# Performance work log

Measured on AMD Instinct MI355X. Metric: run time of the kernel, lower is better.

## Reference

```python
import jax, jax.numpy as jnp
import numpy as np

NUM_HEADS = 8
EPS_OT = 0.05    # self.eps
BETA_T = 1.0     # self.beta_t
N_ITERS = 100    # Sinkhorn max_iter (reference runs all iterations; torch breaks early on convergence)


def setup_inputs() -> dict:
    key = jax.random.key(0)
    ks = jax.random.split(key, 10)
    B, N1, N2 = 16, 256, 576
    dim_t, dim_v, dim_out = 512, 512, 512
    s = 0.02  # conv1d k=1 init scale (stand-in for torch default init)
    f32 = jnp.float32
    return {
        "F_t": jax.random.normal(ks[0], (B, N1, dim_t), f32),
        "F_s": jax.random.normal(ks[1], (B, N2, dim_v), f32),
        # Conv1d(kernel_size=1) weights, squeezed to [out, in]; biases default-on in nn.Conv1d
        "Wq": jax.random.normal(ks[2], (dim_out, dim_t), f32) * s,
        "bq": jnp.zeros((dim_out,), f32),
        "Wk": jax.random.normal(ks[3], (dim_out, dim_v), f32) * s,
        "bk": jnp.zeros((dim_out,), f32),
        "Wv": jax.random.normal(ks[4], (dim_out, dim_v), f32) * s,
        "bv": jnp.zeros((dim_out,), f32),
        "Wp": jax.random.normal(ks[5], (dim_out, dim_out), f32) * s,
        "bp": jnp.zeros((dim_out,), f32),
    }


def sinkhorn_log_exp_sum(C, log_mu, log_nu, eps):
    # C: [BH, N1, N2]; fixed-length log-domain Sinkhorn.
    BH, N1, N2 = C.shape
    u0 = jnp.zeros((BH, N1), C.dtype)
    v0 = jnp.zeros((BH, N2), C.dtype)

    def body(carry, _):
        u, v = carry
        # single K per iteration; both u and v updates use the OLD (u, v), matching torch code
        K = (-C + u[:, :, None] + v[:, None, :]) / eps
        u_new = eps * (log_mu - jax.scipy.special.logsumexp(K, axis=2)) + u
        v_new = eps * (log_nu - jax.scipy.special.logsumexp(K, axis=1)) + v
        return (u_new, v_new), None

    (u, v), _ = jax.lax.scan(jax.checkpoint(body), (u0, v0), None, length=N_ITERS)
    return jnp.exp((-C + u[:, :, None] + v[:, None, :]) / eps)


def _l2norm(x, eps=1e-12):
    return x / jnp.maximum(jnp.linalg.norm(x, axis=-1, keepdims=True), eps)


def reference(F_t, F_s, Wq, bq, Wk, bk, Wv, bv, Wp, bp):
    B, N1, _ = F_t.shape
    N2 = F_s.shape[1]
    H = NUM_HEADS
    dim_out = Wq.shape[0]
    hd = dim_out // H

    # Conv1d(kernel=1) == pointwise linear over channel dim
    q = (F_t @ Wq.T + bq).reshape(B, N1, H, hd)
    k = (F_s @ Wk.T + bk).reshape(B, N2, H, hd)
    v = (F_s @ Wv.T + bv).reshape(B, N2, H, hd)

    q = _l2norm(q)
    k = _l2norm(k)

    sim = jnp.einsum('bnkc,bmkc->bknm', q, k) * BETA_T  # [B,H,N1,N2]
    wdist = (1.0 - sim).reshape(B * H, N1, N2)
    sim_f = sim.reshape(B * H, N1, N2)

    log_mu = jnp.log(jnp.asarray(1.0 / N1 + 1e-8, sim.dtype))
    log_nu = jnp.log(jnp.asarray(1.0 / N2 + 1e-8, sim.dtype))
    T = sinkhorn_log_exp_sum(wdist, log_mu, log_nu, EPS_OT)

    score_map = (N1 * N2 * sim_f * T).reshape(B, H, N1, N2)  # attn_drop = identity (p=0)
    F_t_a = jnp.einsum('bknm,bmkc->bnkc', score_map, v).reshape(B, N1, dim_out)
    F_t_a = F_t_a @ Wp.T + bp
    # torch: F_t_a / F_t_a.norm(dim=-1, keepdim=True)  (plain division, no eps clamp)
    F_t_a = F_t_a / jnp.linalg.norm(F_t_a, axis=-1, keepdims=True)
    return F_t_a  # proj_drop = identity (p=0)
```

## Files before the change

### kernel.cpp

```cpp
#include <hip/hip_runtime.h>
#include <math.h>

#define EPS_OT 0.05f
#define INV_EPS 20.0f

typedef unsigned short ushort_t;
typedef __attribute__((ext_vector_type(8))) short short8;
typedef __attribute__((ext_vector_type(4))) float f32x4;
union Pk { uint4 u; short8 s; };

__device__ __forceinline__ unsigned int f2bf(float f) {
  unsigned int u = __float_as_uint(f);
  return (u + 0x7FFFu + ((u >> 16) & 1u)) >> 16;
}
__device__ __forceinline__ float bf2f(unsigned int u) { return __uint_as_float(u << 16); }

__device__ __forceinline__ void bar_lds() {
  asm volatile("s_waitcnt lgkmcnt(0)" ::: "memory");
  __builtin_amdgcn_s_barrier();
  asm volatile("" ::: "memory");
}

__global__ __launch_bounds__(256) void pack_k(const float* __restrict__ F_t,
                                              const float* __restrict__ F_s,
                                              const float* __restrict__ Wq,
                                              const float* __restrict__ Wk,
                                              const float* __restrict__ Wv,
                                              const float* __restrict__ Wp,
                                              ushort_t* __restrict__ Fth, ushort_t* __restrict__ Ftl,
                                              ushort_t* __restrict__ Fsh, ushort_t* __restrict__ Fsl,
                                              ushort_t* __restrict__ Wqh, ushort_t* __restrict__ Wql,
                                              ushort_t* __restrict__ Wkh, ushort_t* __restrict__ Wkl,
                                              ushort_t* __restrict__ Wvh, ushort_t* __restrict__ Wvl,
                                              ushort_t* __restrict__ Wph) {
  const int blk = blockIdx.x;
  const float* src; ushort_t* dh; ushort_t* dl; size_t off;
  if (blk < 2048)      { src = F_t; dh = Fth; dl = Ftl; off = (size_t)blk * 1024; }
  else if (blk < 6656) { src = F_s; dh = Fsh; dl = Fsl; off = (size_t)(blk - 2048) * 1024; }
  else if (blk < 6912) { src = Wq;  dh = Wqh; dl = Wql; off = (size_t)(blk - 6656) * 1024; }
  else if (blk < 7168) { src = Wk;  dh = Wkh; dl = Wkl; off = (size_t)(blk - 6912) * 1024; }
  else if (blk < 7424) { src = Wv;  dh = Wvh; dl = Wvl; off = (size_t)(blk - 7168) * 1024; }
  else                 { src = Wp;  dh = Wph; dl = nullptr; off = (size_t)(blk - 7424) * 1024; }
  const size_t i = off + (size_t)threadIdx.x * 4;
  float4 f = *(const float4*)(src + i);
  unsigned int h0 = f2bf(f.x), h1 = f2bf(f.y), h2 = f2bf(f.z), h3 = f2bf(f.w);
  uint2 hh; hh.x = h0 | (h1 << 16); hh.y = h2 | (h3 << 16);
  *(uint2*)(dh + i) = hh;
  if (dl) {
    uint2 ll;
    ll.x = f2bf(f.x - bf2f(h0)) | (f2bf(f.y - bf2f(h1)) << 16);
    ll.y = f2bf(f.z - bf2f(h2)) | (f2bf(f.w - bf2f(h3)) << 16);
    *(uint2*)(dl + i) = ll;
  }
}

#define GEMM_HL_BODY()                                                                      \
  f32x4 acc[4] = {};                                                                        \
  for (int k0 = 0; k0 < 512; k0 += 64) {                                                    \
    uint4 a0 = *(const uint4*)(Xp_h + k0), a1 = *(const uint4*)(Xp_h + k0 + 8);             \
    uint4 b0 = *(const uint4*)(Xp_l + k0), b1 = *(const uint4*)(Xp_l + k0 + 8);             \
    uint4 c0 = *(const uint4*)(Wp_h + k0), c1 = *(const uint4*)(Wp_h + k0 + 8);             \
    uint4 d0 = *(const uint4*)(Wp_l + k0), d1 = *(const uint4*)(Wp_l + k0 + 8);             \
    __syncthreads();                                                                        \
    *(uint4*)&Xh[r][cg * 16] = a0; *(uint4*)&Xh[r][cg * 16 + 8] = a1;                       \
    *(uint4*)&Xl[r][cg * 16] = b0; *(uint4*)&Xl[r][cg * 16 + 8] = b1;                       \
    *(uint4*)&Wh[r][cg * 16] = c0; *(uint4*)&Wh[r][cg * 16 + 8] = c1;                       \
    *(uint4*)&Wl[r][cg * 16] = d0; *(uint4*)&Wl[r][cg * 16 + 8] = d1;                       \
    __syncthreads();                                                                        \
    _Pragma("unroll") for (int kst = 0; kst < 2; ++kst) {                                   \
      short8 ah = *(const short8*)&Xh[16 * w + li][kst * 32 + 8 * lg];                      \
      short8 al = *(const short8*)&Xl[16 * w + li][kst * 32 + 8 * lg];                      \
      _Pragma("unroll") for (int nt = 0; nt < 4; ++nt) {                                    \
        short8 bh = *(const short8*)&Wh[nt * 16 + li][kst * 32 + 8 * lg];                   \
        short8 bl = *(const short8*)&Wl[nt * 16 + li][kst * 32 + 8 * lg];                   \
        acc[nt] = __builtin_amdgcn_mfma_f32_16x16x32_bf16(ah, bh, acc[nt], 0, 0, 0);        \
        acc[nt] = __builtin_amdgcn_mfma_f32_16x16x32_bf16(ah, bl, acc[nt], 0, 0, 0);        \
        acc[nt] = __builtin_amdgcn_mfma_f32_16x16x32_bf16(al, bh, acc[nt], 0, 0, 0);        \
      }                                                                                     \
    }                                                                                       \
  }

#define GEMM_PL_BODY()                                                                      \
  f32x4 acc[4] = {};                                                                        \
  for (int k0 = 0; k0 < 512; k0 += 64) {                                                    \
    uint4 a0 = *(const uint4*)(Xp_h + k0), a1 = *(const uint4*)(Xp_h + k0 + 8);             \
    uint4 c0 = *(const uint4*)(Wp_h + k0), c1 = *(const uint4*)(Wp_h + k0 + 8);             \
    __syncthreads();                                                                        \
    *(uint4*)&Xh[r][cg * 16] = a0; *(uint4*)&Xh[r][cg * 16 + 8] = a1;                       \
    *(uint4*)&Wh[r][cg * 16] = c0; *(uint4*)&Wh[r][cg * 16 + 8] = c1;                       \
    __syncthreads();                                                                        \
    _Pragma("unroll") for (int kst = 0; kst < 2; ++kst) {                                   \
      short8 ah = *(const short8*)&Xh[16 * w + li][kst * 32 + 8 * lg];                      \
      _Pragma("unroll") for (int nt = 0; nt < 4; ++nt) {                                    \
        short8 bh = *(const short8*)&Wh[nt * 16 + li][kst * 32 + 8 * lg];                   \
        acc[nt] = __builtin_amdgcn_mfma_f32_16x16x32_bf16(ah, bh, acc[nt], 0, 0, 0);        \
      }                                                                                     \
    }                                                                                       \
  }

__global__ __launch_bounds__(256) void gemmnorm2_k(const ushort_t* __restrict__ Xg_h,
                                                   const ushort_t* __restrict__ Xg_l,
                                                   const ushort_t* __restrict__ Wg_h,
                                                   const ushort_t* __restrict__ Wg_l,
                                                   const float* __restrict__ bias,
                                                   ushort_t* __restrict__ oh,
                                                   ushort_t* __restrict__ ol, int Nn) {
  __shared__ ushort_t Xh[64][72], Xl[64][72], Wh[64][72], Wl[64][72];
  const int tid = threadIdx.x;
  const int w = tid >> 6, l = tid & 63, li = l & 15, lg = l >> 4;
  const int r = tid >> 2, cg = tid & 3;
  const int m0 = blockIdx.x << 6;
  const int h = blockIdx.y, n0 = h << 6;
  const ushort_t* Xp_h = Xg_h + (size_t)(m0 + r) * 512 + cg * 16;
  const ushort_t* Xp_l = Xg_l + (size_t)(m0 + r) * 512 + cg * 16;
  const ushort_t* Wp_h = Wg_h + (size_t)(n0 + r) * 512 + cg * 16;
  const ushort_t* Wp_l = Wg_l + (size_t)(n0 + r) * 512 + cg * 16;
  GEMM_HL_BODY()
  float v[4][4];
  float ss[4] = {0.f, 0.f, 0.f, 0.f};
#pragma unroll
  for (int nt = 0; nt < 4; ++nt) {
    float bb = bias[n0 + nt * 16 + li];
#pragma unroll
    for (int reg = 0; reg < 4; ++reg) {
      float y = acc[nt][reg] + bb;
      v[nt][reg] = y;
      ss[reg] = fmaf(y, y, ss[reg]);
    }
  }
#pragma unroll
  for (int off = 1; off < 16; off <<= 1)
#pragma unroll
    for (int reg = 0; reg < 4; ++reg) ss[reg] += __shfl_xor(ss[reg], off, 64);
  const int b = m0 / Nn;
  const int nbase = m0 - b * Nn;
  const size_t base = ((size_t)(b * 8 + h) * Nn + nbase + 16 * w + 4 * lg) * 64;
#pragma unroll
  for (int reg = 0; reg < 4; ++reg) {
    float inv = 1.0f / fmaxf(sqrtf(ss[reg]), 1e-12f);
#pragma unroll
    for (int nt = 0; nt < 4; ++nt) {
      float y = v[nt][reg] * inv;
      unsigned int hi = f2bf(y);
      size_t idx = base + (size_t)reg * 64 + nt * 16 + li;
      oh[idx] = (ushort_t)hi;
      ol[idx] = (ushort_t)f2bf(y - bf2f(hi));
    }
  }
}

__global__ __launch_bounds__(256) void gemmtrans2_k(const ushort_t* __restrict__ Xg_h,
                                                    const ushort_t* __restrict__ Wg_h,
                                                    const float* __restrict__ bias,
                                                    ushort_t* __restrict__ vt) {
  __shared__ ushort_t Xh[64][72], Wh[64][72];
  __shared__ ushort_t Vs[64 * 73];
  const int tid = threadIdx.x;
  const int w = tid >> 6, l = tid & 63, li = l & 15, lg = l >> 4;
  const int r = tid >> 2, cg = tid & 3;
  const int m0 = blockIdx.x << 6;
  const int h = blockIdx.y, n0 = h << 6;
  const ushort_t* Xp_h = Xg_h + (size_t)(m0 + r) * 512 + cg * 16;
  const ushort_t* Wp_h = Wg_h + (size_t)(n0 + r) * 512 + cg * 16;
  GEMM_PL_BODY()
#pragma unroll
  for (int nt = 0; nt < 4; ++nt) {
    float bb = bias[n0 + nt * 16 + li];
#pragma unroll
    for (int reg = 0; reg < 4; ++reg)
      Vs[(16 * w + 4 * lg + reg) * 73 + nt * 16 + li] = (ushort_t)f2bf(acc[nt][reg] + bb);
  }
  __syncthreads();
  const int a9 = m0 >> 6;
  const int b = a9 / 9;
  const int nbase = m0 - b * 576;
  const int s = b * 8 + h;
  const int c = tid >> 2, q4 = tid & 3;
  ushort_t tmp[16];
#pragma unroll
  for (int jj = 0; jj < 16; ++jj) tmp[jj] = Vs[(q4 * 16 + jj) * 73 + c];
  ushort_t* op = vt + ((size_t)s * 64 + c) * 576 + nbase + q4 * 16;
  *(uint4*)op = *(uint4*)&tmp[0];
  *(uint4*)(op + 8) = *(uint4*)&tmp[8];
}

__global__ __launch_bounds__(256) void gemmplain_k(const ushort_t* __restrict__ Xg_h,
                                                   const ushort_t* __restrict__ Wg_h,
                                                   const float* __restrict__ bias,
                                                   float* __restrict__ Y) {
  __shared__ ushort_t Xh[64][72], Wh[64][72];
  const int tid = threadIdx.x;
  const int w = tid >> 6, l = tid & 63, li = l & 15, lg = l >> 4;
  const int r = tid >> 2, cg = tid & 3;
  const int m0 = blockIdx.x << 6, n0 = blockIdx.y << 6;
  const ushort_t* Xp_h = Xg_h + (size_t)(m0 + r) * 512 + cg * 16;
  const ushort_t* Wp_h = Wg_h + (size_t)(n0 + r) * 512 + cg * 16;
  GEMM_PL_BODY()
#pragma unroll
  for (int nt = 0; nt < 4; ++nt) {
    float bb = bias[n0 + nt * 16 + li];
#pragma unroll
    for (int reg = 0; reg < 4; ++reg)
      Y[(size_t)(m0 + 16 * w + 4 * lg + reg) * 512 + n0 + nt * 16 + li] = acc[nt][reg] + bb;
  }
}

__global__ __launch_bounds__(256) void simE2_k(const ushort_t* __restrict__ qh,
                                               const ushort_t* __restrict__ ql,
                                               const ushort_t* __restrict__ kh,
                                               const ushort_t* __restrict__ kl,
                                               ushort_t* __restrict__ E) {
  const int s = blockIdx.x, i0 = blockIdx.y << 6, j0 = blockIdx.z << 6;
  const int tid = threadIdx.x;
  const int w = tid >> 6, l = tid & 63, li = l & 15, lg = l >> 4;
  const size_t qoff = ((size_t)s * 256 + i0 + 16 * w + li) * 64 + 8 * lg;
  short8 aH0 = *(const short8*)(qh + qoff), aH1 = *(const short8*)(qh + qoff + 32);
  short8 aL0 = *(const short8*)(ql + qoff), aL1 = *(const short8*)(ql + qoff + 32);
  f32x4 acc[4] = {};
#pragma unroll
  for (int nt = 0; nt < 4; ++nt) {
    const size_t koff = ((size_t)s * 576 + j0 + nt * 16 + li) * 64 + 8 * lg;
    short8 bH0 = *(const short8*)(kh + koff), bH1 = *(const short8*)(kh + koff + 32);
    short8 bL0 = *(const short8*)(kl + koff), bL1 = *(const short8*)(kl + koff + 32);
    acc[nt] = __builtin_amdgcn_mfma_f32_16x16x32_bf16(aH0, bH0, acc[nt], 0, 0, 0);
    acc[nt] = __builtin_amdgcn_mfma_f32_16x16x32_bf16(aH1, bH1, acc[nt], 0, 0, 0);
    acc[nt] = __builtin_amdgcn_mfma_f32_16x16x32_bf16(aH0, bL0, acc[nt], 0, 0, 0);
    acc[nt] = __builtin_amdgcn_mfma_f32_16x16x32_bf16(aH1, bL1, acc[nt], 0, 0, 0);
    acc[nt] = __builtin_amdgcn_mfma_f32_16x16x32_bf16(aL0, bH0, acc[nt], 0, 0, 0);
    acc[nt] = __builtin_amdgcn_mfma_f32_16x16x32_bf16(aL1, bH1, acc[nt], 0, 0, 0);
  }
  ushort_t* Ep = E + (size_t)s * 147456;
#pragma unroll
  for (int nt = 0; nt < 4; ++nt)
#pragma unroll
    for (int reg = 0; reg < 4; ++reg) {
      float e = __expf((acc[nt][reg] - 1.0f) * INV_EPS);
      Ep[(size_t)(i0 + 16 * w + 4 * lg + reg) * 576 + j0 + nt * 16 + li] = (ushort_t)f2bf(e);
    }
}

#define SK_SMEM 147456

__global__ __launch_bounds__(1024, 1) void sinkhorn11_k(const ushort_t* __restrict__ E,
                                                        float* __restrict__ gA,
                                                        float* __restrict__ gB,
                                                        unsigned long long* __restrict__ gpart,
                                                        float C_mu, float C_nu) {
  extern __shared__ char smem[];
  const int g = blockIdx.x, s = g >> 1, rh = g & 1, pg = g ^ 1;
  const int tid = threadIdx.x, w = tid >> 6, l = tid & 63, li = l & 15, lg = l >> 4;
  unsigned long long* myP = gpart + (size_t)g * 1152;
  const unsigned long long* prP = gpart + (size_t)pg * 1152;

  ushort_t* Elds = (ushort_t*)smem;
  {
    const uint4* Eg = (const uint4*)(E + (size_t)s * 147456 + (size_t)rh * 73728);
    uint4* El4 = (uint4*)Elds;
    for (int idx = tid; idx < 9216; idx += 1024) El4[idx] = Eg[idx];
  }
  __syncthreads();

  const int art = (w & 7) * 16 + li;
  const int akb = (w >> 3) * 9;
  short8 afr[9];
#pragma unroll
  for (int c = 0; c < 9; ++c)
    afr[c] = *(const short8*)(Elds + art * 576 + (akb + c) * 32 + 8 * lg);

  short8 bfr0, bfr1, bfr2, bfr3, bfr4, bfr5, bfr6, bfr7, bfr8, bfr9, bfr10, bfr11;
#define BFR_BUILD(dst, tc, q)                                                  \
  {                                                                            \
    const ushort_t* p = Elds + ((q) * 32 + 8 * lg) * 576 + (tc) * 16 + li;     \
    Pk pk;                                                                     \
    pk.u.x = (unsigned int)p[0]    | ((unsigned int)p[576]  << 16);            \
    pk.u.y = (unsigned int)p[1152] | ((unsigned int)p[1728] << 16);            \
    pk.u.z = (unsigned int)p[2304] | ((unsigned int)p[2880] << 16);            \
    pk.u.w = (unsigned int)p[3456] | ((unsigned int)p[4032] << 16);            \
    dst = pk.s;                                                                \
  }
  BFR_BUILD(bfr0, w, 0) BFR_BUILD(bfr1, w, 1) BFR_BUILD(bfr2, w, 2) BFR_BUILD(bfr3, w, 3)
  BFR_BUILD(bfr4, w + 16, 0) BFR_BUILD(bfr5, w + 16, 1)
  BFR_BUILD(bfr6, w + 16, 2) BFR_BUILD(bfr7, w + 16, 3)
  if (w < 4) {
    BFR_BUILD(bfr8, w + 32, 0) BFR_BUILD(bfr9, w + 32, 1)
    BFR_BUILD(bfr10, w + 32, 2) BFR_BUILD(bfr11, w + 32, 3)
  } else {
    bfr8 = bfr0; bfr9 = bfr1; bfr10 = bfr2; bfr11 = bfr3;
  }
  __syncthreads();

  float* uu = (float*)smem;
  float* vv = uu + 128;
  ushort_t* au = (ushort_t*)(vv + 576);
  ushort_t* bv = au + 128;
  float* rpart = (float*)(au + 768);
  float* cso = rpart + 256;

  if (tid < 128) { uu[tid] = 0.0f; au[tid] = (ushort_t)0x3F80; }
  if (tid < 576) { vv[tid] = 0.0f; bv[tid] = (ushort_t)0x3F80; }
  __syncthreads();

  const int jj = tid - 128;

  for (int t = 0; t < 100; ++t) {
    const int par = t & 1;
    {
      Pk q0, q1, q2, q3;
      q0.u = *(const uint4*)(au + 8 * lg);
      q1.u = *(const uint4*)(au + 32 + 8 * lg);
      q2.u = *(const uint4*)(au + 64 + 8 * lg);
      q3.u = *(const uint4*)(au + 96 + 8 * lg);
#define MV2_TILE(tc, f0, f1, f2, f3)                                                  \
      {                                                                               \
        f32x4 acc2 = {0.f, 0.f, 0.f, 0.f};                                            \
        acc2 = __builtin_amdgcn_mfma_f32_16x16x32_bf16(q0.s, f0, acc2, 0, 0, 0);      \
        acc2 = __builtin_amdgcn_mfma_f32_16x16x32_bf16(q1.s, f1, acc2, 0, 0, 0);      \
        acc2 = __builtin_amdgcn_mfma_f32_16x16x32_bf16(q2.s, f2, acc2, 0, 0, 0);      \
        acc2 = __builtin_amdgcn_mfma_f32_16x16x32_bf16(q3.s, f3, acc2, 0, 0, 0);      \
        if (l < 16) {                                                                 \
          const int col = (tc) * 16 + l;                                              \
          float cs = acc2[0];                                                         \
          cso[col] = cs;                                                              \
          unsigned long long pv = (unsigned long long)__float_as_uint(cs) |           \
                                  ((unsigned long long)(unsigned int)(t + 1) << 32);  \
          __hip_atomic_store(&myP[par * 576 + col], pv, __ATOMIC_RELAXED,             \
                             __HIP_MEMORY_SCOPE_AGENT);                               \
        }                                                                             \
      }
      MV2_TILE(w, bfr0, bfr1, bfr2, bfr3)
      MV2_TILE(w + 16, bfr4, bfr5, bfr6, bfr7)
      if (w < 4) MV2_TILE(w + 32, bfr8, bfr9, bfr10, bfr11)
    }
    {
      f32x4 acc1 = {0.f, 0.f, 0.f, 0.f};
#pragma unroll
      for (int c = 0; c < 9; ++c) {
        Pk bh; bh.u = *(const uint4*)(bv + (akb + c) * 32 + 8 * lg);
        acc1 = __builtin_amdgcn_mfma_f32_16x16x32_bf16(bh.s, afr[c], acc1, 0, 0, 0);
      }
      if (l < 16) rpart[(w >> 3) * 128 + (w & 7) * 16 + l] = acc1[0];
    }
    bar_lds();
    if (tid < 128) {
      float rs = rpart[tid] + rpart[128 + tid];
      float un = C_mu - EPS_OT * __logf(rs);
      uu[tid] = un;
      au[tid] = (ushort_t)f2bf(__expf(fminf(fmaxf(un * INV_EPS, -80.f), 80.f)));
    } else if (tid < 704) {
      const unsigned int tg = (unsigned int)(t + 1);
      unsigned long long p0;
      for (;;) {
        p0 = __hip_atomic_load(&prP[par * 576 + jj], __ATOMIC_RELAXED, __HIP_MEMORY_SCOPE_AGENT);
        if ((unsigned int)(p0 >> 32) == tg) break;
        __builtin_amdgcn_s_sleep(1);
      }
      float tot = cso[jj] + __uint_as_float((unsigned int)p0);
      float vn = C_nu - EPS_OT * __logf(tot);
      vv[jj] = vn;
      bv[jj] = (ushort_t)f2bf(__expf(fminf(fmaxf(vn * INV_EPS, -80.f), 80.f)));
    }
    bar_lds();
  }
  if (rh == 0 && tid >= 128 && tid < 704) {
    unsigned long long p0;
    for (;;) {
      p0 = __hip_atomic_load(&prP[576 + jj], __ATOMIC_RELAXED, __HIP_MEMORY_SCOPE_AGENT);
      if ((unsigned int)(p0 >> 32) == 100u) break;
      __builtin_amdgcn_s_sleep(1);
    }
    float tot = cso[jj] + __uint_as_float((unsigned int)p0);
    vv[jj] = C_nu - EPS_OT * __logf(tot);
  }
  __syncthreads();
  if (tid < 128) gA[(size_t)s * 256 + rh * 128 + tid] = uu[tid] * INV_EPS;
  if (rh == 0 && tid < 576) gB[(size_t)s * 576 + tid] = vv[tid] * INV_EPS + 11.9012851f;
}

__global__ __launch_bounds__(256) void scorev2_k(const ushort_t* __restrict__ E,
                                                 const ushort_t* __restrict__ vt,
                                                 const float* __restrict__ gA,
                                                 const float* __restrict__ gB,
                                                 ushort_t* __restrict__ Y) {
  __shared__ float gBs[576];
  const int s = blockIdx.x, i0 = blockIdx.y << 6;
  const int tid = threadIdx.x;
  const int w = tid >> 6, l = tid & 63, li = l & 15, lg = l >> 4;
  for (int j = tid; j < 576; j += 256) gBs[j] = gB[(size_t)s * 576 + j];
  const float ga = gA[(size_t)s * 256 + i0 + 16 * w + li];
  const ushort_t* Erow = E + (size_t)s * 147456 + (size_t)(i0 + 16 * w + li) * 576;
  f32x4 acc[4] = {};
  __syncthreads();
  for (int kst = 0; kst < 18; ++kst) {
    const int jb = kst * 32 + 8 * lg;
    Pk eu; eu.u = *(const uint4*)(Erow + jb);
    float pv[8];
#pragma unroll
    for (int jj = 0; jj < 8; ++jj) {
      unsigned int us = (unsigned int)(unsigned short)eu.s[jj];
      float e = bf2f(us);
      float le = __logf(e);
      pv[jj] = (1.0f + EPS_OT * le) * __expf(le + ga + gBs[jb + jj]);
    }
    Pk ph, pl;
#pragma unroll
    for (int jj = 0; jj < 8; ++jj) {
      unsigned int h = f2bf(pv[jj]);
      ((unsigned short*)&ph.s)[jj] = (unsigned short)h;
      ((unsigned short*)&pl.s)[jj] = (unsigned short)f2bf(pv[jj] - bf2f(h));
    }
#pragma unroll
    for (int nt = 0; nt < 4; ++nt) {
      Pk vf; vf.u = *(const uint4*)(vt + ((size_t)s * 64 + nt * 16 + li) * 576 + jb);
      acc[nt] = __builtin_amdgcn_mfma_f32_16x16x32_bf16(ph.s, vf.s, acc[nt], 0, 0, 0);
      acc[nt] = __builtin_amdgcn_mfma_f32_16x16x32_bf16(pl.s, vf.s, acc[nt], 0, 0, 0);
    }
  }
  const int b = s >> 3, h = s & 7;
#pragma unroll
  for (int nt = 0; nt < 4; ++nt)
#pragma unroll
    for (int reg = 0; reg < 4; ++reg)
      Y[((size_t)(b * 256 + i0 + 16 * w + 4 * lg + reg) << 9) + (h << 6) + nt * 16 + li] =
          (ushort_t)f2bf(acc[nt][reg]);
}

__global__ __launch_bounds__(256) void rownorm_k(const float* __restrict__ X,
                                                 float* __restrict__ out) {
  const size_t row = blockIdx.x;
  const int tid = threadIdx.x;
  float x0 = X[(row << 9) + tid], x1 = X[(row << 9) + 256 + tid];
  float st = fmaf(x0, x0, x1 * x1);
#pragma unroll
  for (int off = 32; off; off >>= 1) st += __shfl_xor(st, off, 64);
  __shared__ float ps[4];
  if ((tid & 63) == 0) ps[tid >> 6] = st;
  __syncthreads();
  const float inv = 1.0f / sqrtf(ps[0] + ps[1] + ps[2] + ps[3]);
  out[(row << 9) + tid] = x0 * inv;
  out[(row << 9) + 256 + tid] = x1 * inv;
}

extern "C" void kernel_launch(void* const* d_in, const int* in_sizes, int n_in,
                              void* d_out, int out_size, void* d_ws, size_t ws_size,
                              hipStream_t stream) {
  const float* F_t = (const float*)d_in[0];
  const float* F_s = (const float*)d_in[1];
  const float* Wq = (const float*)d_in[2];
  const float* bq = (const float*)d_in[3];
  const float* Wk = (const float*)d_in[4];
  const float* bk = (const float*)d_in[5];
  const float* Wv = (const float*)d_in[6];
  const float* bvb = (const float*)d_in[7];
  const float* Wp = (const float*)d_in[8];
  const float* bp = (const float*)d_in[9];
  float* out = (float*)d_out;

  ushort_t* u0 = (ushort_t*)d_ws;
  ushort_t* Fth = u0;
  ushort_t* Ftl = Fth + 2097152;
  ushort_t* Fsh = Ftl + 2097152;
  ushort_t* Fsl = Fsh + 4718592;
  ushort_t* Wqh = Fsl + 4718592;
  ushort_t* Wql = Wqh + 262144;
  ushort_t* Wkh = Wql + 262144;
  ushort_t* Wkl = Wkh + 262144;
  ushort_t* Wvh = Wkl + 262144;
  ushort_t* Wvl = Wvh + 262144;
  ushort_t* Wph = Wvl + 262144;
  ushort_t* qh = Wph + 262144;
  ushort_t* ql = qh + 2097152;
  ushort_t* kh = ql + 2097152;
  ushort_t* kl = kh + 4718592;
  ushort_t* vt = kl + 4718592;
  ushort_t* Eb = vt + 4718592;
  ushort_t* T0b = Eb + 18874368;
  float* T1 = (float*)(T0b + 2097152);
  float* gA = T1 + 2097152;
  float* gB = gA + 32768;
  unsigned long long* gpart = (unsigned long long*)(gB + 73728);

  const float C_mu = (float)(0.05 * log(1.0 / 256.0 + 1e-8));
  const float C_nu = (float)(0.05 * log(1.0 / 576.0 + 1e-8));

  (void)hipFuncSetAttribute((const void*)sinkhorn11_k,
                            hipFuncAttributeMaxDynamicSharedMemorySize, SK_SMEM);

  pack_k<<<7680, 256, 0, stream>>>(F_t, F_s, Wq, Wk, Wv, Wp, Fth, Ftl, Fsh, Fsl,
                                   Wqh, Wql, Wkh, Wkl, Wvh, Wvl, Wph);
  gemmnorm2_k<<<dim3(64, 8), 256, 0, stream>>>(Fth, Ftl, Wqh, Wql, bq, qh, ql, 256);
  gemmnorm2_k<<<dim3(144, 8), 256, 0, stream>>>(Fsh, Fsl, Wkh, Wkl, bk, kh, kl, 576);
  gemmtrans2_k<<<dim3(144, 8), 256, 0, stream>>>(Fsh, Wvh, bvb, vt);
  simE2_k<<<dim3(128, 4, 9), 256, 0, stream>>>(qh, ql, kh, kl, Eb);
  sinkhorn11_k<<<256, 1024, SK_SMEM, stream>>>(Eb, gA, gB, gpart, C_mu, C_nu);
  scorev2_k<<<dim3(128, 4), 256, 0, stream>>>(Eb, vt, gA, gB, T0b);
  gemmplain_k<<<dim3(64, 8), 256, 0, stream>>>(T0b, Wph, bp, T1);
  rownorm_k<<<4096, 256, 0, stream>>>(T1, out);
}
```

Before: 371.9 us.

## Specialize Sinkhorn waves into row and column roles with double-buffered scalings

The Sinkhorn kernel now splits its waves by role. Waves 0-7 hold full row fragments and compute the u update directly. Waves 8-15 hold the column fragments, plus a small LDS stash for the leftover tiles, and compute the v update along with the cross-block partial exchange. The au/bv scaling vectors are double-buffered, so each iteration needs one barrier instead of two and the separate serial update phase goes away. The cost is that more fragments sit in registers per wave and the polling loops are unrolled across five tiles.

```diff
diff --git a/kernel.cpp b/kernel.cpp
--- a/kernel.cpp
+++ b/kernel.cpp
@@ -241,7 +241,7 @@
 
 #define SK_SMEM 147456
 
-__global__ __launch_bounds__(1024, 1) void sinkhorn11_k(const ushort_t* __restrict__ E,
+__global__ __launch_bounds__(1024, 1) void sinkhorn13_k(const ushort_t* __restrict__ E,
                                                         float* __restrict__ gA,
                                                         float* __restrict__ gB,
                                                         unsigned long long* __restrict__ gpart,
@@ -260,15 +260,10 @@
   }
   __syncthreads();
 
-  const int art = (w & 7) * 16 + li;
-  const int akb = (w >> 3) * 9;
-  short8 afr[9];
-#pragma unroll
-  for (int c = 0; c < 9; ++c)
-    afr[c] = *(const short8*)(Elds + art * 576 + (akb + c) * 32 + 8 * lg);
-
-  short8 bfr0, bfr1, bfr2, bfr3, bfr4, bfr5, bfr6, bfr7, bfr8, bfr9, bfr10, bfr11;
-#define BFR_BUILD(dst, tc, q)                                                  \
+  const int wc = w - 8;
+  short8 frag[18];
+  short8 tfr0, tfr1, tfr2, tfr3;
+#define BFRV(dst, tc, q)                                                       \
   {                                                                            \
     const ushort_t* p = Elds + ((q) * 32 + 8 * lg) * 576 + (tc) * 16 + li;     \
     Pk pk;                                                                     \
@@ -278,100 +273,134 @@
     pk.u.w = (unsigned int)p[3456] | ((unsigned int)p[4032] << 16);            \
     dst = pk.s;                                                                \
   }
-  BFR_BUILD(bfr0, w, 0) BFR_BUILD(bfr1, w, 1) BFR_BUILD(bfr2, w, 2) BFR_BUILD(bfr3, w, 3)
-  BFR_BUILD(bfr4, w + 16, 0) BFR_BUILD(bfr5, w + 16, 1)
-  BFR_BUILD(bfr6, w + 16, 2) BFR_BUILD(bfr7, w + 16, 3)
-  if (w < 4) {
-    BFR_BUILD(bfr8, w + 32, 0) BFR_BUILD(bfr9, w + 32, 1)
-    BFR_BUILD(bfr10, w + 32, 2) BFR_BUILD(bfr11, w + 32, 3)
+  if (w < 8) {
+    const int art = w * 16 + li;
+#pragma unroll
+    for (int c = 0; c < 18; ++c)
+      frag[c] = *(const short8*)(Elds + art * 576 + c * 32 + 8 * lg);
+    tfr0 = frag[0]; tfr1 = frag[0]; tfr2 = frag[0]; tfr3 = frag[0];
   } else {
-    bfr8 = bfr0; bfr9 = bfr1; bfr10 = bfr2; bfr11 = bfr3;
+#pragma unroll
+    for (int j = 0; j < 4; ++j)
+#pragma unroll
+      for (int q = 0; q < 4; ++q) BFRV(frag[j * 4 + q], wc * 4 + j, q)
+    frag[16] = frag[0]; frag[17] = frag[0];
+    if (wc < 4) {
+      BFRV(tfr0, 32 + wc, 0) BFRV(tfr1, 32 + wc, 1)
+      BFRV(tfr2, 32 + wc, 2) BFRV(tfr3, 32 + wc, 3)
+    } else {
+      tfr0 = frag[0]; tfr1 = frag[0]; tfr2 = frag[0]; tfr3 = frag[0];
+    }
   }
   __syncthreads();
 
   float* uu = (float*)smem;
   float* vv = uu + 128;
   ushort_t* au = (ushort_t*)(vv + 576);
-  ushort_t* bv = au + 128;
-  float* rpart = (float*)(au + 768);
-  float* cso = rpart + 256;
+  ushort_t* bv = au + 256;
+  uint4* stash = (uint4*)(bv + 1152);
 
   if (tid < 128) { uu[tid] = 0.0f; au[tid] = (ushort_t)0x3F80; }
   if (tid < 576) { vv[tid] = 0.0f; bv[tid] = (ushort_t)0x3F80; }
+  if (w >= 8 && wc < 4) {
+    Pk t0, t1, t2, t3;
+    t0.s = tfr0; t1.s = tfr1; t2.s = tfr2; t3.s = tfr3;
+    stash[(wc * 4 + 0) * 64 + l] = t0.u;
+    stash[(wc * 4 + 1) * 64 + l] = t1.u;
+    stash[(wc * 4 + 2) * 64 + l] = t2.u;
+    stash[(wc * 4 + 3) * 64 + l] = t3.u;
+  }
   __syncthreads();
 
-  const int jj = tid - 128;
-
   for (int t = 0; t < 100; ++t) {
-    const int par = t & 1;
-    {
+    const int rd = t & 1, wr = rd ^ 1, par = t & 1;
+    if (w < 8) {
+      const ushort_t* bvr = bv + rd * 576;
+      f32x4 acc1 = {0.f, 0.f, 0.f, 0.f};
+#pragma unroll
+      for (int c = 0; c < 18; ++c) {
+        Pk bh; bh.u = *(const uint4*)(bvr + c * 32 + 8 * lg);
+        acc1 = __builtin_amdgcn_mfma_f32_16x16x32_bf16(bh.s, frag[c], acc1, 0, 0, 0);
+      }
+      if (l < 16) {
+        const int row = w * 16 + l;
+        float un = C_mu - EPS_OT * __logf(acc1[0]);
+        uu[row] = un;
+        au[wr * 128 + row] =
+            (ushort_t)f2bf(__expf(fminf(fmaxf(un * INV_EPS, -80.f), 80.f)));
+      }
+    } else {
+      const ushort_t* aur = au + rd * 128;
       Pk q0, q1, q2, q3;
-      q0.u = *(const uint4*)(au + 8 * lg);
-      q1.u = *(const uint4*)(au + 32 + 8 * lg);
-      q2.u = *(const uint4*)(au + 64 + 8 * lg);
-      q3.u = *(const uint4*)(au + 96 + 8 * lg);
-#define MV2_TILE(tc, f0, f1, f2, f3)                                                  \
-      {                                                                               \
-        f32x4 acc2 = {0.f, 0.f, 0.f, 0.f};                                            \
-        acc2 = __builtin_amdgcn_mfma_f32_16x16x32_bf16(q0.s, f0, acc2, 0, 0, 0);      \
-        acc2 = __builtin_amdgcn_mfma_f32_16x16x32_bf16(q1.s, f1, acc2, 0, 0, 0);      \
-        acc2 = __builtin_amdgcn_mfma_f32_16x16x32_bf16(q2.s, f2, acc2, 0, 0, 0);      \
-        acc2 = __builtin_amdgcn_mfma_f32_16x16x32_bf16(q3.s, f3, acc2, 0, 0, 0);      \
-        if (l < 16) {                                                                 \
-          const int col = (tc) * 16 + l;                                              \
-          float cs = acc2[0];                                                         \
-          cso[col] = cs;                                                              \
-          unsigned long long pv = (unsigned long long)__float_as_uint(cs) |           \
-                                  ((unsigned long long)(unsigned int)(t + 1) << 32);  \
-          __hip_atomic_store(&myP[par * 576 + col], pv, __ATOMIC_RELAXED,             \
-                             __HIP_MEMORY_SCOPE_AGENT);                               \
-        }                                                                             \
+      q0.u = *(const uint4*)(aur + 8 * lg);
+      q1.u = *(const uint4*)(aur + 32 + 8 * lg);
+      q2.u = *(const uint4*)(aur + 64 + 8 * lg);
+      q3.u = *(const uint4*)(aur + 96 + 8 * lg);
+      float cs0, cs1, cs2, cs3, cs4 = 0.f;
+#define MV2T(CSV, F0, F1, F2, F3, TC)                                                \
+      {                                                                              \
+        f32x4 a2 = {0.f, 0.f, 0.f, 0.f};                                             \
+        a2 = __builtin_amdgcn_mfma_f32_16x16x32_bf16(q0.s, F0, a2, 0, 0, 0);         \
+        a2 = __builtin_amdgcn_mfma_f32_16x16x32_bf16(q1.s, F1, a2, 0, 0, 0);         \
+        a2 = __builtin_amdgcn_mfma_f32_16x16x32_bf16(q2.s, F2, a2, 0, 0, 0);         \
+        a2 = __builtin_amdgcn_mfma_f32_16x16x32_bf16(q3.s, F3, a2, 0, 0, 0);         \
+        CSV = a2[0];                                                                 \
+        if (l < 16) {                                                                \
+          unsigned long long pv = (unsigned long long)__float_as_uint(CSV) |         \
+                                  ((unsigned long long)(unsigned int)(t + 1) << 32); \
+          __hip_atomic_store(&myP[par * 576 + (TC) * 16 + l], pv, __ATOMIC_RELAXED,  \
+                             __HIP_MEMORY_SCOPE_AGENT);                              \
+        }                                                                            \
       }
-      MV2_TILE(w, bfr0, bfr1, bfr2, bfr3)
-      MV2_TILE(w + 16, bfr4, bfr5, bfr6, bfr7)
-      if (w < 4) MV2_TILE(w + 32, bfr8, bfr9, bfr10, bfr11)
-    }
-    {
-      f32x4 acc1 = {0.f, 0.f, 0.f, 0.f};
-#pragma unroll
-      for (int c = 0; c < 9; ++c) {
-        Pk bh; bh.u = *(const uint4*)(bv + (akb + c) * 32 + 8 * lg);
-        acc1 = __builtin_amdgcn_mfma_f32_16x16x32_bf16(bh.s, afr[c], acc1, 0, 0, 0);
+      MV2T(cs0, frag[0], frag[1], frag[2], frag[3], wc * 4 + 0)
+      MV2T(cs1, frag[4], frag[5], frag[6], frag[7], wc * 4 + 1)
+      MV2T(cs2, frag[8], frag[9], frag[10], frag[11], wc * 4 + 2)
+      MV2T(cs3, frag[12], frag[13], frag[14], frag[15], wc * 4 + 3)
+      if (wc < 4) {
+        Pk s0, s1, s2, s3;
+        s0.u = stash[(wc * 4 + 0) * 64 + l];
+        s1.u = stash[(wc * 4 + 1) * 64 + l];
+        s2.u = stash[(wc * 4 + 2) * 64 + l];
+        s3.u = stash[(wc * 4 + 3) * 64 + l];
+        MV2T(cs4, s0.s, s1.s, s2.s, s3.s, 32 + wc)
       }
-      if (l < 16) rpart[(w >> 3) * 128 + (w & 7) * 16 + l] = acc1[0];
+      if (l < 16) {
+        const unsigned int tg = (unsigned int)(t + 1);
+        unsigned long long p0, p1, p2, p3, p4 = 0;
+        p0 = __hip_atomic_load(&prP[par * 576 + (wc * 4 + 0) * 16 + l],
+                               __ATOMIC_RELAXED, __HIP_MEMORY_SCOPE_AGENT);
+        p1 = __hip_atomic_load(&prP[par * 576 + (wc * 4 + 1) * 16 + l],
+                               __ATOMIC_RELAXED, __HIP_MEMORY_SCOPE_AGENT);
+        p2 = __hip_atomic_load(&prP[par * 576 + (wc * 4 + 2) * 16 + l],
+                               __ATOMIC_RELAXED, __HIP_MEMORY_SCOPE_AGENT);
+        p3 = __hip_atomic_load(&prP[par * 576 + (wc * 4 + 3) * 16 + l],
+                               __ATOMIC_RELAXED, __HIP_MEMORY_SCOPE_AGENT);
+        if (wc < 4)
+          p4 = __hip_atomic_load(&prP[par * 576 + (32 + wc) * 16 + l],
+                                 __ATOMIC_RELAXED, __HIP_MEMORY_SCOPE_AGENT);
+#define VUPD(PV, CSV, TC)                                                              \
+        {                                                                              \
+          while ((unsigned int)((PV) >> 32) != tg) {                                   \
+            __builtin_amdgcn_s_sleep(1);                                               \
+            PV = __hip_atomic_load(&prP[par * 576 + (TC) * 16 + l], __ATOMIC_RELAXED,  \
+                                   __HIP_MEMORY_SCOPE_AGENT);                          \
+          }                                                                            \
+          const int col = (TC) * 16 + l;                                               \
+          float tot = CSV + __uint_as_float((unsigned int)(PV));                       \
+          float vn = C_nu - EPS_OT * __logf(tot);                                      \
+          vv[col] = vn;                                                                \
+          bv[wr * 576 + col] =                                                         \
+              (ushort_t)f2bf(__expf(fminf(fmaxf(vn * INV_EPS, -80.f), 80.f)));         \
+        }
+        VUPD(p0, cs0, wc * 4 + 0)
+        VUPD(p1, cs1, wc * 4 + 1)
+        VUPD(p2, cs2, wc * 4 + 2)
+        VUPD(p3, cs3, wc * 4 + 3)
+        if (wc < 4) VUPD(p4, cs4, 32 + wc)
+      }
     }
     bar_lds();
-    if (tid < 128) {
-      float rs = rpart[tid] + rpart[128 + tid];
-      float un = C_mu - EPS_OT * __logf(rs);
-      uu[tid] = un;
-      au[tid] = (ushort_t)f2bf(__expf(fminf(fmaxf(un * INV_EPS, -80.f), 80.f)));
-    } else if (tid < 704) {
-      const unsigned int tg = (unsigned int)(t + 1);
-      unsigned long long p0;
-      for (;;) {
-        p0 = __hip_atomic_load(&prP[par * 576 + jj], __ATOMIC_RELAXED, __HIP_MEMORY_SCOPE_AGENT);
-        if ((unsigned int)(p0 >> 32) == tg) break;
-        __builtin_amdgcn_s_sleep(1);
-      }
-      float tot = cso[jj] + __uint_as_float((unsigned int)p0);
-      float vn = C_nu - EPS_OT * __logf(tot);
-      vv[jj] = vn;
-      bv[jj] = (ushort_t)f2bf(__expf(fminf(fmaxf(vn * INV_EPS, -80.f), 80.f)));
-    }
-    bar_lds();
-  }
-  if (rh == 0 && tid >= 128 && tid < 704) {
-    unsigned long long p0;
-    for (;;) {
-      p0 = __hip_atomic_load(&prP[576 + jj], __ATOMIC_RELAXED, __HIP_MEMORY_SCOPE_AGENT);
-      if ((unsigned int)(p0 >> 32) == 100u) break;
-      __builtin_amdgcn_s_sleep(1);
-    }
-    float tot = cso[jj] + __uint_as_float((unsigned int)p0);
-    vv[jj] = C_nu - EPS_OT * __logf(tot);
-  }
-  __syncthreads();
+  }
   if (tid < 128) gA[(size_t)s * 256 + rh * 128 + tid] = uu[tid] * INV_EPS;
   if (rh == 0 && tid < 576) gB[(size_t)s * 576 + tid] = vv[tid] * INV_EPS + 11.9012851f;
 }
@@ -482,7 +511,7 @@
   const float C_mu = (float)(0.05 * log(1.0 / 256.0 + 1e-8));
   const float C_nu = (float)(0.05 * log(1.0 / 576.0 + 1e-8));
 
-  (void)hipFuncSetAttribute((const void*)sinkhorn11_k,
+  (void)hipFuncSetAttribute((const void*)sinkhorn13_k,
                             hipFuncAttributeMaxDynamicSharedMemorySize, SK_SMEM);
 
   pack_k<<<7680, 256, 0, stream>>>(F_t, F_s, Wq, Wk, Wv, Wp, Fth, Ftl, Fsh, Fsl,
@@ -491,7 +520,7 @@
   gemmnorm2_k<<<dim3(144, 8), 256, 0, stream>>>(Fsh, Fsl, Wkh, Wkl, bk, kh, kl, 576);
   gemmtrans2_k<<<dim3(144, 8), 256, 0, stream>>>(Fsh, Wvh, bvb, vt);
   simE2_k<<<dim3(128, 4, 9), 256, 0, stream>>>(qh, ql, kh, kl, Eb);
-  sinkhorn11_k<<<256, 1024, SK_SMEM, stream>>>(Eb, gA, gB, gpart, C_mu, C_nu);
+  sinkhorn13_k<<<256, 1024, SK_SMEM, stream>>>(Eb, gA, gB, gpart, C_mu, C_nu);
   scorev2_k<<<dim3(128, 4), 256, 0, stream>>>(Eb, vt, gA, gB, T0b);
   gemmplain_k<<<dim3(64, 8), 256, 0, stream>>>(T0b, Wph, bp, T1);
   rownorm_k<<<4096, 256, 0, stream>>>(T1, out);
```

After: 498.9 us. 34.1% more time.

## Software-pipeline Sinkhorn partner exchange to overlap cross-block wait with next matvec

Applied to the files above, without the earlier changes.

Restructures the Sinkhorn iteration loop so each block computes and publishes its column partial sums for the next step before waiting on the partner block's previous-step partials. This hides the cross-block atomic handoff latency behind MFMA work. To support it, the exchange buffer becomes a 4-slot ring, the column-sum scratch is double-buffered, and each block zeroes its own slots at kernel start. The cost is a larger global scratch area and a possible race between that zeroing and partner reads of stale tags.

```diff
diff --git a/kernel.cpp b/kernel.cpp
--- a/kernel.cpp
+++ b/kernel.cpp
@@ -241,7 +241,7 @@
 
 #define SK_SMEM 147456
 
-__global__ __launch_bounds__(1024, 1) void sinkhorn11_k(const ushort_t* __restrict__ E,
+__global__ __launch_bounds__(1024, 1) void sinkhorn14_k(const ushort_t* __restrict__ E,
                                                         float* __restrict__ gA,
                                                         float* __restrict__ gB,
                                                         unsigned long long* __restrict__ gpart,
@@ -249,8 +249,11 @@
   extern __shared__ char smem[];
   const int g = blockIdx.x, s = g >> 1, rh = g & 1, pg = g ^ 1;
   const int tid = threadIdx.x, w = tid >> 6, l = tid & 63, li = l & 15, lg = l >> 4;
-  unsigned long long* myP = gpart + (size_t)g * 1152;
-  const unsigned long long* prP = gpart + (size_t)pg * 1152;
+  unsigned long long* myP = gpart + (size_t)g * 2304;
+  const unsigned long long* prP = gpart + (size_t)pg * 2304;
+
+  for (int i = tid; i < 2304; i += 1024)
+    __hip_atomic_store(&myP[i], 0ull, __ATOMIC_RELAXED, __HIP_MEMORY_SCOPE_AGENT);
 
   ushort_t* Elds = (ushort_t*)smem;
   {
@@ -300,76 +303,92 @@
   if (tid < 576) { vv[tid] = 0.0f; bv[tid] = (ushort_t)0x3F80; }
   __syncthreads();
 
-  const int jj = tid - 128;
-
-  for (int t = 0; t < 100; ++t) {
-    const int par = t & 1;
-    {
-      Pk q0, q1, q2, q3;
-      q0.u = *(const uint4*)(au + 8 * lg);
-      q1.u = *(const uint4*)(au + 32 + 8 * lg);
-      q2.u = *(const uint4*)(au + 64 + 8 * lg);
-      q3.u = *(const uint4*)(au + 96 + 8 * lg);
-#define MV2_TILE(tc, f0, f1, f2, f3)                                                  \
-      {                                                                               \
-        f32x4 acc2 = {0.f, 0.f, 0.f, 0.f};                                            \
-        acc2 = __builtin_amdgcn_mfma_f32_16x16x32_bf16(q0.s, f0, acc2, 0, 0, 0);      \
-        acc2 = __builtin_amdgcn_mfma_f32_16x16x32_bf16(q1.s, f1, acc2, 0, 0, 0);      \
-        acc2 = __builtin_amdgcn_mfma_f32_16x16x32_bf16(q2.s, f2, acc2, 0, 0, 0);      \
-        acc2 = __builtin_amdgcn_mfma_f32_16x16x32_bf16(q3.s, f3, acc2, 0, 0, 0);      \
-        if (l < 16) {                                                                 \
-          const int col = (tc) * 16 + l;                                              \
-          float cs = acc2[0];                                                         \
-          cso[col] = cs;                                                              \
-          unsigned long long pv = (unsigned long long)__float_as_uint(cs) |           \
-                                  ((unsigned long long)(unsigned int)(t + 1) << 32);  \
-          __hip_atomic_store(&myP[par * 576 + col], pv, __ATOMIC_RELAXED,             \
-                             __HIP_MEMORY_SCOPE_AGENT);                               \
-        }                                                                             \
+  float* csoW; unsigned int tagv; int slotv;
+#define MV2_TILE(tc, f0, f1, f2, f3)                                                \
+  {                                                                                 \
+    f32x4 a2 = {0.f, 0.f, 0.f, 0.f};                                                \
+    a2 = __builtin_amdgcn_mfma_f32_16x16x32_bf16(q0.s, f0, a2, 0, 0, 0);            \
+    a2 = __builtin_amdgcn_mfma_f32_16x16x32_bf16(q1.s, f1, a2, 0, 0, 0);            \
+    a2 = __builtin_amdgcn_mfma_f32_16x16x32_bf16(q2.s, f2, a2, 0, 0, 0);            \
+    a2 = __builtin_amdgcn_mfma_f32_16x16x32_bf16(q3.s, f3, a2, 0, 0, 0);            \
+    if (l < 16) {                                                                   \
+      const int col = (tc) * 16 + l;                                                \
+      csoW[col] = a2[0];                                                            \
+      unsigned long long pv = (unsigned long long)__float_as_uint(a2[0]) |          \
+                              ((unsigned long long)tagv << 32);                     \
+      __hip_atomic_store(&myP[slotv * 576 + col], pv, __ATOMIC_RELAXED,             \
+                         __HIP_MEMORY_SCOPE_AGENT);                                 \
+    }                                                                               \
+  }
+#define MV2_ALL()                                                                   \
+  {                                                                                 \
+    Pk q0, q1, q2, q3;                                                              \
+    q0.u = *(const uint4*)(au + 8 * lg);                                            \
+    q1.u = *(const uint4*)(au + 32 + 8 * lg);                                       \
+    q2.u = *(const uint4*)(au + 64 + 8 * lg);                                       \
+    q3.u = *(const uint4*)(au + 96 + 8 * lg);                                       \
+    MV2_TILE(w, bfr0, bfr1, bfr2, bfr3)                                             \
+    MV2_TILE(w + 16, bfr4, bfr5, bfr6, bfr7)                                        \
+    if (w < 4) MV2_TILE(w + 32, bfr8, bfr9, bfr10, bfr11)                           \
+  }
+#define MV1_ALL()                                                                   \
+  {                                                                                 \
+    f32x4 acc1 = {0.f, 0.f, 0.f, 0.f};                                              \
+    _Pragma("unroll") for (int c = 0; c < 9; ++c) {                                 \
+      Pk bh; bh.u = *(const uint4*)(bv + (akb + c) * 32 + 8 * lg);                  \
+      acc1 = __builtin_amdgcn_mfma_f32_16x16x32_bf16(bh.s, afr[c], acc1, 0, 0, 0);  \
+    }                                                                               \
+    if (l < 16) rpart[(w >> 3) * 128 + (w & 7) * 16 + l] = acc1[0];                 \
+  }
+#define U_UPD()                                                                     \
+  if (tid < 128) {                                                                  \
+    float rs = rpart[tid] + rpart[128 + tid];                                       \
+    float un = C_mu - EPS_OT * __logf(rs);                                          \
+    uu[tid] = un;                                                                   \
+    au[tid] = (ushort_t)f2bf(__expf(fminf(fmaxf(un * INV_EPS, -80.f), 80.f)));      \
+  }
+
+  csoW = cso; tagv = 1u; slotv = 0;
+  MV2_ALL()
+  MV1_ALL()
+  bar_lds();
+  U_UPD()
+  bar_lds();
+
+  for (int t = 1; t < 100; ++t) {
+    csoW = cso + (t & 1) * 576; tagv = (unsigned int)(t + 1); slotv = t & 3;
+    MV2_ALL()
+    if (tid < 576) {
+      const unsigned int tg = (unsigned int)t;
+      const unsigned long long* sp = &prP[((t - 1) & 3) * 576 + tid];
+      unsigned long long p0 =
+          __hip_atomic_load(sp, __ATOMIC_RELAXED, __HIP_MEMORY_SCOPE_AGENT);
+      while ((unsigned int)(p0 >> 32) != tg) {
+        __builtin_amdgcn_s_sleep(1);
+        p0 = __hip_atomic_load(sp, __ATOMIC_RELAXED, __HIP_MEMORY_SCOPE_AGENT);
       }
-      MV2_TILE(w, bfr0, bfr1, bfr2, bfr3)
-      MV2_TILE(w + 16, bfr4, bfr5, bfr6, bfr7)
-      if (w < 4) MV2_TILE(w + 32, bfr8, bfr9, bfr10, bfr11)
-    }
-    {
-      f32x4 acc1 = {0.f, 0.f, 0.f, 0.f};
-#pragma unroll
-      for (int c = 0; c < 9; ++c) {
-        Pk bh; bh.u = *(const uint4*)(bv + (akb + c) * 32 + 8 * lg);
-        acc1 = __builtin_amdgcn_mfma_f32_16x16x32_bf16(bh.s, afr[c], acc1, 0, 0, 0);
-      }
-      if (l < 16) rpart[(w >> 3) * 128 + (w & 7) * 16 + l] = acc1[0];
+      float tot = cso[((t - 1) & 1) * 576 + tid] + __uint_as_float((unsigned int)p0);
+      float vn = C_nu - EPS_OT * __logf(tot);
+      vv[tid] = vn;
+      bv[tid] = (ushort_t)f2bf(__expf(fminf(fmaxf(vn * INV_EPS, -80.f), 80.f)));
     }
     bar_lds();
-    if (tid < 128) {
-      float rs = rpart[tid] + rpart[128 + tid];
-      float un = C_mu - EPS_OT * __logf(rs);
-      uu[tid] = un;
-      au[tid] = (ushort_t)f2bf(__expf(fminf(fmaxf(un * INV_EPS, -80.f), 80.f)));
-    } else if (tid < 704) {
-      const unsigned int tg = (unsigned int)(t + 1);
-      unsigned long long p0;
-      for (;;) {
-        p0 = __hip_atomic_load(&prP[par * 576 + jj], __ATOMIC_RELAXED, __HIP_MEMORY_SCOPE_AGENT);
-        if ((unsigned int)(p0 >> 32) == tg) break;
-        __builtin_amdgcn_s_sleep(1);
-      }
-      float tot = cso[jj] + __uint_as_float((unsigned int)p0);
-      float vn = C_nu - EPS_OT * __logf(tot);
-      vv[jj] = vn;
-      bv[jj] = (ushort_t)f2bf(__expf(fminf(fmaxf(vn * INV_EPS, -80.f), 80.f)));
-    }
+    MV1_ALL()
     bar_lds();
-  }
-  if (rh == 0 && tid >= 128 && tid < 704) {
-    unsigned long long p0;
-    for (;;) {
-      p0 = __hip_atomic_load(&prP[576 + jj], __ATOMIC_RELAXED, __HIP_MEMORY_SCOPE_AGENT);
-      if ((unsigned int)(p0 >> 32) == 100u) break;
+    U_UPD()
+    bar_lds();
+  }
+
+  if (rh == 0 && tid < 576) {
+    const unsigned long long* sp = &prP[3 * 576 + tid];
+    unsigned long long p0 =
+        __hip_atomic_load(sp, __ATOMIC_RELAXED, __HIP_MEMORY_SCOPE_AGENT);
+    while ((unsigned int)(p0 >> 32) != 100u) {
       __builtin_amdgcn_s_sleep(1);
-    }
-    float tot = cso[jj] + __uint_as_float((unsigned int)p0);
-    vv[jj] = C_nu - EPS_OT * __logf(tot);
+      p0 = __hip_atomic_load(sp, __ATOMIC_RELAXED, __HIP_MEMORY_SCOPE_AGENT);
+    }
+    float tot = cso[576 + tid] + __uint_as_float((unsigned int)p0);
+    vv[tid] = C_nu - EPS_OT * __logf(tot);
   }
   __syncthreads();
   if (tid < 128) gA[(size_t)s * 256 + rh * 128 + tid] = uu[tid] * INV_EPS;
@@ -482,7 +501,7 @@
   const float C_mu = (float)(0.05 * log(1.0 / 256.0 + 1e-8));
   const float C_nu = (float)(0.05 * log(1.0 / 576.0 + 1e-8));
 
-  (void)hipFuncSetAttribute((const void*)sinkhorn11_k,
+  (void)hipFuncSetAttribute((const void*)sinkhorn14_k,
                             hipFuncAttributeMaxDynamicSharedMemorySize, SK_SMEM);
 
   pack_k<<<7680, 256, 0, stream>>>(F_t, F_s, Wq, Wk, Wv, Wp, Fth, Ftl, Fsh, Fsl,
@@ -491,7 +510,7 @@
   gemmnorm2_k<<<dim3(144, 8), 256, 0, stream>>>(Fsh, Fsl, Wkh, Wkl, bk, kh, kl, 576);
   gemmtrans2_k<<<dim3(144, 8), 256, 0, stream>>>(Fsh, Wvh, bvb, vt);
   simE2_k<<<dim3(128, 4, 9), 256, 0, stream>>>(qh, ql, kh, kl, Eb);
-  sinkhorn11_k<<<256, 1024, SK_SMEM, stream>>>(Eb, gA, gB, gpart, C_mu, C_nu);
+  sinkhorn14_k<<<256, 1024, SK_SMEM, stream>>>(Eb, gA, gB, gpart, C_mu, C_nu);
   scorev2_k<<<dim3(128, 4), 256, 0, stream>>>(Eb, vt, gA, gB, T0b);
   gemmplain_k<<<dim3(64, 8), 256, 0, stream>>>(T0b, Wph, bp, T1);
   rownorm_k<<<4096, 256, 0, stream>>>(T1, out);
```

New measurement: 384.4 us. +3.4%, slower.
